# Kernel tuning notes

Hardware: AMD Instinct MI355X
Metric: run time of the kernel (lower is better)

The kernel has to match this reference:

```python
import jax, jax.numpy as jnp
import numpy as np

# dims: batch B, seq T, model C, expert hidden H, num experts E, top-k K
B, T, C, H, E, K = 4, 1024, 1024, 1024, 8, 2


def _swiglu(x):
    a, b = jnp.split(x, 2, axis=-1)
    return jax.nn.silu(a) * b


def setup_inputs() -> dict:
    key = jax.random.key(0)
    ks = jax.random.split(key, 6)
    s = 0.02
    x = jax.random.normal(ks[0], (B, T, C), jnp.float32)
    # weights stored [in, out] (transpose of torch Linear layout; same math y = x @ W)
    w_shared_in = jax.random.normal(ks[1], (C, 2 * H), jnp.float32) * s
    w_shared_out = jax.random.normal(ks[2], (H, C), jnp.float32) * s
    w1_shared = jax.random.normal(ks[3], (C, 2 * H), jnp.float32) * s
    w2 = jax.random.normal(ks[4], (E, H, C), jnp.float32) * s  # stacked routed_w2
    w_gate = jax.random.normal(ks[5], (C, E), jnp.float32) * s
    gate_bias = jnp.zeros((E,), jnp.float32)  # buffer, updated only in training
    return {
        "x": x,
        "w_shared_in": w_shared_in,
        "w_shared_out": w_shared_out,
        "w1_shared": w1_shared,
        "w2": w2,
        "w_gate": w_gate,
        "gate_bias": gate_bias,
    }


def reference(x, w_shared_in, w_shared_out, w1_shared, w2, w_gate, gate_bias):
    Bx, Tx, Cx = x.shape
    S = Bx * Tx
    fx = x.reshape(S, Cx)  # [S, C]

    # shared expert: SwiGLU MLP
    shared_out = _swiglu(fx @ w_shared_in) @ w_shared_out  # [S, C]

    # router: softmax(top-k) over biased logits
    logits = fx @ w_gate + gate_bias  # [S, E]
    probs = jax.nn.softmax(logits, axis=-1)
    top_val, top_idx = jax.lax.top_k(probs, K)  # [S, K]

    # dense dispatch-weight matrix [S, E] (zero where expert not selected)
    wdense = jnp.zeros((S, E), probs.dtype).at[
        jnp.arange(S)[:, None], top_idx
    ].add(top_val)

    # routed experts share w1_shared, so the SwiGLU hidden is identical for all
    # experts; compute it once for every token, then apply per-expert w2.
    hid = _swiglu(fx @ w1_shared)  # [S, H]
    routed_out = jnp.zeros_like(shared_out)
    for e in range(E):  # small fixed expert count
        routed_out = routed_out + wdense[:, e:e + 1] * (hid @ w2[e])

    return (shared_out + routed_out).reshape(Bx, Tx, Cx)
```

## Files before the change

kernel.cpp:

```cpp
#include <hip/hip_runtime.h>
#include <stdint.h>

typedef __attribute__((ext_vector_type(4))) float f32x4;
typedef __attribute__((ext_vector_type(8))) short s16x8;

static constexpr int S_TOK = 4096;
static constexpr int CDIM  = 1024;
static constexpr int HDIM  = 1024;
static constexpr int H2    = 2048;
static constexpr int NEXP  = 8;

#define BK 32
#define MAXRT2 40

__device__ __forceinline__ unsigned short f2bf(float f) {
  union { float f; uint32_t u; } c; c.f = f;
  uint32_t u = c.u;
  u += 0x7fffu + ((u >> 16) & 1u);
  return (unsigned short)(u >> 16);
}

__device__ __forceinline__ float bf2f(unsigned short u) {
  return __uint_as_float(((uint32_t)u) << 16);
}

__device__ __forceinline__ void gload16(const void* g, void* l) {
  __builtin_amdgcn_global_load_lds(
      (const __attribute__((address_space(1))) void*)g,
      (__attribute__((address_space(3))) void*)l, 16, 0, 0);
}

__global__ void cast_bf16_kernel(const float* __restrict__ src,
                                 unsigned short* __restrict__ dst, int n4) {
  int i = blockIdx.x * blockDim.x + threadIdx.x;
  const int st = gridDim.x * blockDim.x;
  for (; i < n4; i += st) {
    float4 v = reinterpret_cast<const float4*>(src)[i];
    ushort4 o;
    o.x = f2bf(v.x); o.y = f2bf(v.y); o.z = f2bf(v.z); o.w = f2bf(v.w);
    reinterpret_cast<ushort4*>(dst)[i] = o;
  }
}

__global__ void wprep_in_kernel(const float* __restrict__ wsi, const float* __restrict__ w1s,
                                unsigned short* __restrict__ dst) {
  __shared__ float t[32][33];
  const float* src = blockIdx.z ? w1s : wsi;
  const int halfoff = blockIdx.z ? 2048 : 0;
  const int r0 = blockIdx.y * 32;
  const int c0 = blockIdx.x * 32;
  const int tid = threadIdx.x;
#pragma unroll
  for (int i = 0; i < 4; ++i) {
    int idx = tid + i * 256;
    int r = idx >> 5, c = idx & 31;
    t[r][c] = src[(size_t)(r0 + r) * H2 + c0 + c];
  }
  __syncthreads();
#pragma unroll
  for (int i = 0; i < 4; ++i) {
    int idx = tid + i * 256;
    int r = idx >> 5, c = idx & 31;
    const int ccol = c0 + r;
    const int part = ccol >> 10, h = ccol & 1023;
    const int drow = halfoff + (h & 15) + ((h >> 4) << 5) + (part << 4);
    dst[(size_t)drow * CDIM + r0 + c] = f2bf(t[c][r]);
  }
}

__global__ void transpose_cast_kernel(const float* __restrict__ src,
                                      unsigned short* __restrict__ dst,
                                      int R, int Cc) {
  __shared__ float t[32][33];
  const size_t zoff = (size_t)blockIdx.z * R * Cc;
  src += zoff; dst += zoff;
  const int r0 = blockIdx.y * 32;
  const int c0 = blockIdx.x * 32;
  const int tid = threadIdx.x;
#pragma unroll
  for (int i = 0; i < 4; ++i) {
    int idx = tid + i * 256;
    int r = idx >> 5, c = idx & 31;
    t[r][c] = src[(size_t)(r0 + r) * Cc + c0 + c];
  }
  __syncthreads();
#pragma unroll
  for (int i = 0; i < 4; ++i) {
    int idx = tid + i * 256;
    int r = idx >> 5, c = idx & 31;
    dst[(size_t)(c0 + r) * R + r0 + c] = f2bf(t[c][r]);
  }
}

__global__ void router_kernel(const float* __restrict__ x, const float* __restrict__ wg,
                              const float* __restrict__ gb,
                              int2* __restrict__ ti_e, float2* __restrict__ ti_w) {
  const int l = threadIdx.x & 63;
  const int wid = threadIdx.x >> 6;
  const int s = blockIdx.x * 4 + wid;
  const float* xr = x + (size_t)s * CDIM;
  float acc[NEXP];
#pragma unroll
  for (int e = 0; e < NEXP; ++e) acc[e] = 0.f;
  for (int c = l; c < CDIM; c += 64) {
    float xv = xr[c];
    const float* wr_ = wg + (size_t)c * NEXP;
#pragma unroll
    for (int e = 0; e < NEXP; ++e) acc[e] += xv * wr_[e];
  }
#pragma unroll
  for (int e = 0; e < NEXP; ++e) {
#pragma unroll
    for (int off = 32; off > 0; off >>= 1) acc[e] += __shfl_xor(acc[e], off);
    acc[e] += gb[e];
  }
  float m = acc[0];
#pragma unroll
  for (int e = 1; e < NEXP; ++e) m = fmaxf(m, acc[e]);
  float ex[NEXP], sum = 0.f;
#pragma unroll
  for (int e = 0; e < NEXP; ++e) { ex[e] = __expf(acc[e] - m); sum += ex[e]; }
  int i0 = 0;
#pragma unroll
  for (int e = 1; e < NEXP; ++e) if (acc[e] > acc[i0]) i0 = e;
  int i1 = (i0 == 0) ? 1 : 0;
#pragma unroll
  for (int e = 0; e < NEXP; ++e) {
    if (e == i0) continue;
    if (acc[e] > acc[i1]) i1 = e;
  }
  if (l == 0) {
    const float inv = 1.f / sum;
    ti_e[s] = make_int2(i0, i1);
    ti_w[s] = make_float2(ex[i0] * inv, ex[i1] * inv);
  }
}

__global__ __launch_bounds__(1024) void build_kernel(
    const int2* __restrict__ ti_e,
    int* __restrict__ cnt, int* __restrict__ offs,
    int* __restrict__ gidx, int2* __restrict__ ti_slot) {
  __shared__ int gcnt[64][NEXP];
  __shared__ int gbase[64][NEXP];
  __shared__ int eoff[NEXP];
  const int tid = threadIdx.x;
  const int wid = tid >> 6, lane = tid & 63;

  for (int p = 0; p < 4; ++p) {
    const int g = p * 16 + wid;
    const int2 e = ti_e[g * 64 + lane];
#pragma unroll
    for (int ex = 0; ex < NEXP; ++ex) {
      uint64_t b0 = __ballot(e.x == ex);
      uint64_t b1 = __ballot(e.y == ex);
      if (lane == 0) gcnt[g][ex] = __popcll(b0) + __popcll(b1);
    }
  }
  __syncthreads();
  if (tid < NEXP) {
    const int ex = tid;
    int a = 0;
    for (int g = 0; g < 64; ++g) { gbase[g][ex] = a; a += gcnt[g][ex]; }
    eoff[ex] = a;
  }
  __syncthreads();
  if (tid == 0) {
    int a = 0;
#pragma unroll
    for (int ex = 0; ex < NEXP; ++ex) {
      const int c = eoff[ex];
      offs[ex] = a; cnt[ex] = c; eoff[ex] = a; a += c;
    }
    offs[NEXP] = a;
  }
  __syncthreads();
  for (int p = 0; p < 4; ++p) {
    const int g = p * 16 + wid;
    const int s = g * 64 + lane;
    const int2 e = ti_e[s];
    const uint64_t below = (lane == 0) ? 0ull : (~0ull >> (64 - lane));
    const uint64_t beloweq = below | (1ull << lane);
    int slot0 = 0, slot1 = 0;
#pragma unroll
    for (int ex = 0; ex < NEXP; ++ex) {
      uint64_t b0 = __ballot(e.x == ex);
      uint64_t b1 = __ballot(e.y == ex);
      const int base = gbase[g][ex];
      if (e.x == ex) slot0 = base + __popcll(b0 & below) + __popcll(b1 & below);
      if (e.y == ex) slot1 = base + __popcll(b0 & beloweq) + __popcll(b1 & below);
    }
    ti_slot[s] = make_int2(slot0, slot1);
    gidx[eoff[e.x] + slot0] = s;
    gidx[eoff[e.y] + slot1] = s;
  }
}

__global__ __launch_bounds__(256, 4) void gemm1_kernel(
    const unsigned short* __restrict__ xb, const unsigned short* __restrict__ w12i,
    unsigned short* __restrict__ Hs, unsigned short* __restrict__ Hr) {
  __shared__ unsigned short As[128 * BK];
  __shared__ unsigned short Bs[128 * BK];
  const int tid = threadIdx.x;
  const int l = tid & 63, wid = tid >> 6;
  const int wr = wid >> 1, wc = wid & 1;
  const int lr = l & 15, lk = (l >> 4) << 3;
  const int hw = blockIdx.y * gridDim.x + blockIdx.x;
  const int logical = (hw & 7) * 128 + (hw >> 3);
  const int m0 = (logical >> 5) * 128;
  const int n0 = (logical & 31) * 128;
  f32x4 acc[4][4] = {};
  const unsigned short* ga0 = xb + (size_t)(m0 + (tid >> 2)) * CDIM + ((tid & 3) << 3);
  const unsigned short* ga1 = ga0 + (size_t)64 * CDIM;
  const unsigned short* gb0 = w12i + (size_t)(n0 + (tid >> 2)) * CDIM + ((tid & 3) << 3);
  const unsigned short* gb1 = gb0 + (size_t)64 * CDIM;

  for (int k0 = 0; k0 < 1024; k0 += BK) {
    gload16(ga0 + k0, As + tid * 8);
    gload16(ga1 + k0, As + 2048 + tid * 8);
    gload16(gb0 + k0, Bs + tid * 8);
    gload16(gb1 + k0, Bs + 2048 + tid * 8);
    __syncthreads();
    s16x8 a[4], b[4];
#pragma unroll
    for (int fm = 0; fm < 4; ++fm)
      a[fm] = *reinterpret_cast<const s16x8*>(As + (wr * 64 + fm * 16 + lr) * BK + lk);
#pragma unroll
    for (int fn = 0; fn < 4; ++fn)
      b[fn] = *reinterpret_cast<const s16x8*>(Bs + (wc * 64 + fn * 16 + lr) * BK + lk);
#pragma unroll
    for (int fm = 0; fm < 4; ++fm)
#pragma unroll
      for (int fn = 0; fn < 4; ++fn)
        acc[fm][fn] = __builtin_amdgcn_mfma_f32_16x16x32_bf16(a[fm], b[fn], acc[fm][fn], 0, 0, 0);
    __syncthreads();
  }

  unsigned short* Hbuf = (n0 < 2048) ? Hs : Hr;
  const int rb = m0 + wr * 64 + ((l >> 4) << 2);
  const int hb0 = ((n0 & 2047) >> 1) + wc * 32;
#pragma unroll
  for (int fm = 0; fm < 4; ++fm)
#pragma unroll
    for (int j = 0; j < 2; ++j)
#pragma unroll
      for (int r = 0; r < 4; ++r) {
        float a = acc[fm][2 * j][r];
        float b = acc[fm][2 * j + 1][r];
        float hv = (a / (1.f + __expf(-a))) * b;
        Hbuf[(size_t)(rb + fm * 16 + r) * HDIM + hb0 + j * 16 + lr] = f2bf(hv);
      }
}

__global__ __launch_bounds__(512) void gemm2_kernel(
    const unsigned short* __restrict__ Hs, const unsigned short* __restrict__ Hr,
    const unsigned short* __restrict__ wso_t, const unsigned short* __restrict__ w2t,
    const int* __restrict__ cnt, const int* __restrict__ offs, const int* __restrict__ gidx,
    float* __restrict__ out, unsigned short* __restrict__ Eout) {
  __shared__ unsigned short SA[4][2][4096];
  __shared__ unsigned short SB[4][2][4096];
  const int tid = threadIdx.x;
  const int l = tid & 63, wid = tid >> 6;
  const int wm = wid >> 2, wn = wid & 3;
  const int lr = l & 15;
  const int hi8 = (l >> 4) << 3;
  const int wnh = wn >> 1;
  const int wno = (wn & 1) << 6;
  const int hw = blockIdx.y * gridDim.x + blockIdx.x;
  const int logical = (hw & 7) * 28 + (hw >> 3);
  const int gx = logical >> 2;
  const int n0 = (logical & 3) * 256;
  f32x4 acc[8][4] = {};

  const int srow = tid >> 2;
  const int cs = (((tid & 3) ^ ((tid >> 3) & 3)) << 3);

  const unsigned short *pa0, *pa1, *pb0, *pb1;
  int e = 0, cnte = 0, mt = 0, base = 0;
  const bool dense = (gx < 16);
  if (dense) {
    const int m0 = gx * 256;
    pa0 = Hs + (size_t)(m0 + srow) * HDIM + cs;
    pa1 = pa0 + (size_t)128 * HDIM;
    pb0 = wso_t + (size_t)(n0 + srow) * HDIM + cs;
    pb1 = pb0 + (size_t)128 * HDIM;
  } else {
    int t = gx - 16;
    bool found = false;
#pragma unroll
    for (int ee = 0; ee < NEXP; ++ee) {
      int c = cnt[ee];
      int nt = (c + 255) >> 8;
      if (!found) {
        if (t < nt) { e = ee; cnte = c; found = true; }
        else t -= nt;
      }
    }
    if (!found) return;
    mt = t;
    base = offs[e];
    const int r0 = mt * 256 + srow;
    const int tok0 = gidx[base + min(r0, cnte - 1)];
    const int tok1 = gidx[base + min(r0 + 128, cnte - 1)];
    pa0 = Hr + (size_t)tok0 * HDIM + cs;
    pa1 = Hr + (size_t)tok1 * HDIM + cs;
    pb0 = w2t + (size_t)e * CDIM * HDIM + (size_t)(n0 + srow) * HDIM + cs;
    pb1 = pb0 + (size_t)128 * HDIM;
  }

  const int t8 = tid * 8;
#pragma unroll
  for (int s = 0; s < 3; ++s) {
    const int kk = s * 32;
    gload16(pa0 + kk, &SA[s][0][t8]);
    gload16(pa1 + kk, &SA[s][1][t8]);
    gload16(pb0 + kk, &SB[s][0][t8]);
    gload16(pb1 + kk, &SB[s][1][t8]);
  }

  for (int s = 0; s < 32; ++s) {
    if (s < 30)       asm volatile("s_waitcnt vmcnt(8)" ::: "memory");
    else if (s == 30) asm volatile("s_waitcnt vmcnt(4)" ::: "memory");
    else              asm volatile("s_waitcnt vmcnt(0)" ::: "memory");
    __builtin_amdgcn_s_barrier();
    asm volatile("" ::: "memory");
    const int c = s & 3;
    const unsigned short* A_ = &SA[c][wm][0];
    const unsigned short* B_ = &SB[c][wnh][0];
    s16x8 a[8], b[4];
#pragma unroll
    for (int f = 0; f < 8; ++f) {
      const int r = f * 16 + lr;
      a[f] = *reinterpret_cast<const s16x8*>(&A_[r * 32 + (hi8 ^ (((r >> 1) & 3) << 3))]);
    }
#pragma unroll
    for (int j = 0; j < 4; ++j) {
      const int r = wno + j * 16 + lr;
      b[j] = *reinterpret_cast<const s16x8*>(&B_[r * 32 + (hi8 ^ (((r >> 1) & 3) << 3))]);
    }
    const int c3 = (s + 3) & 3;
    const int kk = (s + 3) * 32;
    const bool st = (s <= 28);
    if (st) gload16(pa0 + kk, &SA[c3][0][t8]);
    __builtin_amdgcn_s_setprio(1);
#pragma unroll
    for (int f = 0; f < 4; ++f) {
      acc[f][0] = __builtin_amdgcn_mfma_f32_16x16x32_bf16(a[f], b[0], acc[f][0], 0, 0, 0);
      acc[f][1] = __builtin_amdgcn_mfma_f32_16x16x32_bf16(a[f], b[1], acc[f][1], 0, 0, 0);
    }
    __builtin_amdgcn_s_setprio(0);
    if (st) gload16(pa1 + kk, &SA[c3][1][t8]);
    __builtin_amdgcn_s_setprio(1);
#pragma unroll
    for (int f = 0; f < 4; ++f) {
      acc[f][2] = __builtin_amdgcn_mfma_f32_16x16x32_bf16(a[f], b[2], acc[f][2], 0, 0, 0);
      acc[f][3] = __builtin_amdgcn_mfma_f32_16x16x32_bf16(a[f], b[3], acc[f][3], 0, 0, 0);
    }
    __builtin_amdgcn_s_setprio(0);
    if (st) gload16(pb0 + kk, &SB[c3][0][t8]);
    __builtin_amdgcn_s_setprio(1);
#pragma unroll
    for (int f = 0; f < 4; ++f) {
      acc[4 + f][0] = __builtin_amdgcn_mfma_f32_16x16x32_bf16(a[4 + f], b[0], acc[4 + f][0], 0, 0, 0);
      acc[4 + f][1] = __builtin_amdgcn_mfma_f32_16x16x32_bf16(a[4 + f], b[1], acc[4 + f][1], 0, 0, 0);
    }
    __builtin_amdgcn_s_setprio(0);
    if (st) gload16(pb1 + kk, &SB[c3][1][t8]);
    __builtin_amdgcn_s_setprio(1);
#pragma unroll
    for (int f = 0; f < 4; ++f) {
      acc[4 + f][2] = __builtin_amdgcn_mfma_f32_16x16x32_bf16(a[4 + f], b[2], acc[4 + f][2], 0, 0, 0);
      acc[4 + f][3] = __builtin_amdgcn_mfma_f32_16x16x32_bf16(a[4 + f], b[3], acc[4 + f][3], 0, 0, 0);
    }
    __builtin_amdgcn_s_setprio(0);
  }

  const int rloc0 = wm * 128 + ((l >> 4) << 2);
  const int cb = n0 + wn * 64 + lr;
  if (dense) {
    const int rb = gx * 256 + rloc0;
#pragma unroll
    for (int fm = 0; fm < 8; ++fm)
#pragma unroll
      for (int fn = 0; fn < 4; ++fn)
#pragma unroll
        for (int r = 0; r < 4; ++r)
          out[(size_t)(rb + fm * 16 + r) * CDIM + cb + fn * 16] = acc[fm][fn][r];
  } else {
#pragma unroll
    for (int fm = 0; fm < 8; ++fm)
#pragma unroll
      for (int fn = 0; fn < 4; ++fn)
#pragma unroll
        for (int r = 0; r < 4; ++r) {
          const int rloc = mt * 256 + rloc0 + fm * 16 + r;
          if (rloc < cnte)
            Eout[(size_t)(base + rloc) * CDIM + cb + fn * 16] = f2bf(acc[fm][fn][r]);
        }
  }
}

__global__ void scatter_kernel(float* __restrict__ out, const unsigned short* __restrict__ Eout,
                               const int2* __restrict__ ti_e, const int2* __restrict__ ti_slot,
                               const float2* __restrict__ ti_w, const int* __restrict__ offs) {
  const int total = S_TOK * (CDIM / 8);
  int i = blockIdx.x * blockDim.x + threadIdx.x;
  const int st = gridDim.x * blockDim.x;
  for (; i < total; i += st) {
    const int s = i >> 7;
    const int j = (i & 127) << 3;
    const int2 e = ti_e[s];
    const int2 sl = ti_slot[s];
    const float2 wv = ti_w[s];
    const int p0 = offs[e.x] + sl.x;
    const int p1 = offs[e.y] + sl.y;
    const ushort4* e0 = reinterpret_cast<const ushort4*>(Eout + (size_t)p0 * CDIM + j);
    const ushort4* e1 = reinterpret_cast<const ushort4*>(Eout + (size_t)p1 * CDIM + j);
    float* op = out + (size_t)s * CDIM + j;
#pragma unroll
    for (int q = 0; q < 2; ++q) {
      ushort4 a = e0[q], b = e1[q];
      float4 o = reinterpret_cast<float4*>(op)[q];
      o.x += wv.x * bf2f(a.x) + wv.y * bf2f(b.x);
      o.y += wv.x * bf2f(a.y) + wv.y * bf2f(b.y);
      o.z += wv.x * bf2f(a.z) + wv.y * bf2f(b.z);
      o.w += wv.x * bf2f(a.w) + wv.y * bf2f(b.w);
      reinterpret_cast<float4*>(op)[q] = o;
    }
  }
}

extern "C" void kernel_launch(void* const* d_in, const int* in_sizes, int n_in,
                              void* d_out, int out_size, void* d_ws, size_t ws_size,
                              hipStream_t stream) {
  (void)in_sizes; (void)n_in; (void)out_size; (void)ws_size;
  const float* x   = (const float*)d_in[0];
  const float* wsi = (const float*)d_in[1];
  const float* wso = (const float*)d_in[2];
  const float* w1s = (const float*)d_in[3];
  const float* w2  = (const float*)d_in[4];
  const float* wg  = (const float*)d_in[5];
  const float* gb  = (const float*)d_in[6];
  float* out = (float*)d_out;

  char* w = (char*)d_ws;
  auto alloc = [&](size_t bytes) {
    char* p = w; w += (bytes + 255) & ~(size_t)255; return p;
  };
  unsigned short* xb    = (unsigned short*)alloc((size_t)S_TOK * CDIM * 2);
  unsigned short* w12i  = (unsigned short*)alloc((size_t)2 * H2 * CDIM * 2);
  unsigned short* wso_t = (unsigned short*)alloc((size_t)CDIM * HDIM * 2);
  unsigned short* w2t   = (unsigned short*)alloc((size_t)NEXP * CDIM * HDIM * 2);
  unsigned short* Hs    = (unsigned short*)alloc((size_t)S_TOK * HDIM * 2);
  unsigned short* Hr    = (unsigned short*)alloc((size_t)S_TOK * HDIM * 2);
  unsigned short* Eout  = (unsigned short*)alloc((size_t)2 * S_TOK * CDIM * 2);
  int2*   ti_e   = (int2*)alloc((size_t)S_TOK * 8);
  int2*   ti_slot= (int2*)alloc((size_t)S_TOK * 8);
  float2* ti_w   = (float2*)alloc((size_t)S_TOK * 8);
  int*    cnt    = (int*)alloc(64);
  int*    offs   = (int*)alloc(64);
  int*    gidx   = (int*)alloc((size_t)2 * S_TOK * 4);

  router_kernel<<<S_TOK / 4, 256, 0, stream>>>(x, wg, gb, ti_e, ti_w);
  build_kernel<<<1, 1024, 0, stream>>>(ti_e, cnt, offs, gidx, ti_slot);

  cast_bf16_kernel<<<2048, 256, 0, stream>>>(x, xb, S_TOK * CDIM / 4);
  wprep_in_kernel<<<dim3(H2 / 32, CDIM / 32, 2), 256, 0, stream>>>(wsi, w1s, w12i);
  transpose_cast_kernel<<<dim3(CDIM / 32, HDIM / 32, 1), 256, 0, stream>>>(wso, wso_t, HDIM, CDIM);
  transpose_cast_kernel<<<dim3(CDIM / 32, HDIM / 32, NEXP), 256, 0, stream>>>(w2, w2t, HDIM, CDIM);

  gemm1_kernel<<<dim3(32, 32), 256, 0, stream>>>(xb, w12i, Hs, Hr);

  gemm2_kernel<<<dim3(16 + MAXRT2, CDIM / 256), 512, 0, stream>>>(
      Hs, Hr, wso_t, w2t, cnt, offs, gidx, out, Eout);

  scatter_kernel<<<2048, 256, 0, stream>>>(out, Eout, ti_e, ti_slot, ti_w, offs);
}
```

Measured before the change: 128.7 us.

## Fuse x cast into router, merge weight prep kernels, store shared output as bf16

The x-to-bf16 cast now happens inside the router kernel, which reads x with float4 loads, so x is read once instead of twice. The three weight transpose/cast kernels are merged into one flat-grid prep kernel to cut launch count. The shared-expert GEMM result is written to a bf16 buffer instead of fp32 out, so scatter writes out without first reading it. This trades less memory traffic and fewer launches for an extra bf16 rounding on the shared-expert output.

```diff
diff --git a/kernel.cpp b/kernel.cpp
--- a/kernel.cpp
+++ b/kernel.cpp
@@ -10,7 +10,6 @@
 static constexpr int H2    = 2048;
 static constexpr int NEXP  = 8;
 
-#define BK 32
 #define MAXRT2 40
 
 __device__ __forceinline__ unsigned short f2bf(float f) {
@@ -30,83 +29,93 @@
       (__attribute__((address_space(3))) void*)l, 16, 0, 0);
 }
 
-__global__ void cast_bf16_kernel(const float* __restrict__ src,
-                                 unsigned short* __restrict__ dst, int n4) {
-  int i = blockIdx.x * blockDim.x + threadIdx.x;
-  const int st = gridDim.x * blockDim.x;
-  for (; i < n4; i += st) {
-    float4 v = reinterpret_cast<const float4*>(src)[i];
-    ushort4 o;
-    o.x = f2bf(v.x); o.y = f2bf(v.y); o.z = f2bf(v.z); o.w = f2bf(v.w);
-    reinterpret_cast<ushort4*>(dst)[i] = o;
-  }
-}
-
-__global__ void wprep_in_kernel(const float* __restrict__ wsi, const float* __restrict__ w1s,
-                                unsigned short* __restrict__ dst) {
+__global__ __launch_bounds__(256) void prep_kernel(
+    const float* __restrict__ wsi, const float* __restrict__ w1s,
+    const float* __restrict__ wso, const float* __restrict__ w2,
+    unsigned short* __restrict__ w12i, unsigned short* __restrict__ wso_t,
+    unsigned short* __restrict__ w2t) {
   __shared__ float t[32][33];
-  const float* src = blockIdx.z ? w1s : wsi;
-  const int halfoff = blockIdx.z ? 2048 : 0;
-  const int r0 = blockIdx.y * 32;
-  const int c0 = blockIdx.x * 32;
+  const int b = blockIdx.x;
   const int tid = threadIdx.x;
+
+  if (b < 4096) {
+    const float* src = (b >= 2048) ? w1s : wsi;
+    const int halfoff = (b >= 2048) ? 2048 : 0;
+    const int rem = b & 2047;
+    const int r0 = (rem >> 6) * 32;
+    const int c0 = (rem & 63) * 32;
+#pragma unroll
+    for (int i = 0; i < 4; ++i) {
+      int idx = tid + i * 256;
+      int r = idx >> 5, c = idx & 31;
+      t[r][c] = src[(size_t)(r0 + r) * H2 + c0 + c];
+    }
+    __syncthreads();
+#pragma unroll
+    for (int i = 0; i < 4; ++i) {
+      int idx = tid + i * 256;
+      int r = idx >> 5, c = idx & 31;
+      const int ccol = c0 + r;
+      const int part = ccol >> 10, h = ccol & 1023;
+      const int drow = halfoff + (h & 15) + ((h >> 4) << 5) + (part << 4);
+      w12i[(size_t)drow * CDIM + r0 + c] = f2bf(t[c][r]);
+    }
+    return;
+  }
+  const float* src;
+  unsigned short* dst;
+  int bx, by;
+  if (b < 5120) {
+    const int b3 = b - 4096;
+    src = wso; dst = wso_t; by = b3 >> 5; bx = b3 & 31;
+  } else {
+    const int b4 = b - 5120;
+    const int z = b4 >> 10;
+    const int rem = b4 & 1023;
+    src = w2 + (size_t)z * HDIM * CDIM;
+    dst = w2t + (size_t)z * HDIM * CDIM;
+    by = rem >> 5; bx = rem & 31;
+  }
+  const int r0 = by * 32, c0 = bx * 32;
 #pragma unroll
   for (int i = 0; i < 4; ++i) {
     int idx = tid + i * 256;
     int r = idx >> 5, c = idx & 31;
-    t[r][c] = src[(size_t)(r0 + r) * H2 + c0 + c];
+    t[r][c] = src[(size_t)(r0 + r) * CDIM + c0 + c];
   }
   __syncthreads();
 #pragma unroll
   for (int i = 0; i < 4; ++i) {
     int idx = tid + i * 256;
     int r = idx >> 5, c = idx & 31;
-    const int ccol = c0 + r;
-    const int part = ccol >> 10, h = ccol & 1023;
-    const int drow = halfoff + (h & 15) + ((h >> 4) << 5) + (part << 4);
-    dst[(size_t)drow * CDIM + r0 + c] = f2bf(t[c][r]);
-  }
-}
-
-__global__ void transpose_cast_kernel(const float* __restrict__ src,
-                                      unsigned short* __restrict__ dst,
-                                      int R, int Cc) {
-  __shared__ float t[32][33];
-  const size_t zoff = (size_t)blockIdx.z * R * Cc;
-  src += zoff; dst += zoff;
-  const int r0 = blockIdx.y * 32;
-  const int c0 = blockIdx.x * 32;
-  const int tid = threadIdx.x;
-#pragma unroll
-  for (int i = 0; i < 4; ++i) {
-    int idx = tid + i * 256;
-    int r = idx >> 5, c = idx & 31;
-    t[r][c] = src[(size_t)(r0 + r) * Cc + c0 + c];
-  }
-  __syncthreads();
-#pragma unroll
-  for (int i = 0; i < 4; ++i) {
-    int idx = tid + i * 256;
-    int r = idx >> 5, c = idx & 31;
-    dst[(size_t)(c0 + r) * R + r0 + c] = f2bf(t[c][r]);
+    dst[(size_t)(c0 + r) * HDIM + r0 + c] = f2bf(t[c][r]);
   }
 }
 
 __global__ void router_kernel(const float* __restrict__ x, const float* __restrict__ wg,
                               const float* __restrict__ gb,
-                              int2* __restrict__ ti_e, float2* __restrict__ ti_w) {
+                              int2* __restrict__ ti_e, float2* __restrict__ ti_w,
+                              unsigned short* __restrict__ xb) {
   const int l = threadIdx.x & 63;
   const int wid = threadIdx.x >> 6;
   const int s = blockIdx.x * 4 + wid;
   const float* xr = x + (size_t)s * CDIM;
+  unsigned short* xbr = xb + (size_t)s * CDIM;
   float acc[NEXP];
 #pragma unroll
   for (int e = 0; e < NEXP; ++e) acc[e] = 0.f;
-  for (int c = l; c < CDIM; c += 64) {
-    float xv = xr[c];
-    const float* wr_ = wg + (size_t)c * NEXP;
-#pragma unroll
-    for (int e = 0; e < NEXP; ++e) acc[e] += xv * wr_[e];
+#pragma unroll
+  for (int c4 = 0; c4 < CDIM / 4; c4 += 64) {
+    const int i4 = c4 + l;
+    const float4 xv = reinterpret_cast<const float4*>(xr)[i4];
+    ushort4 o;
+    o.x = f2bf(xv.x); o.y = f2bf(xv.y); o.z = f2bf(xv.z); o.w = f2bf(xv.w);
+    reinterpret_cast<ushort4*>(xbr)[i4] = o;
+    const float* wr_ = wg + (size_t)i4 * 4 * NEXP;
+#pragma unroll
+    for (int e = 0; e < NEXP; ++e)
+      acc[e] += xv.x * wr_[e] + xv.y * wr_[e + NEXP] +
+                xv.z * wr_[e + 2 * NEXP] + xv.w * wr_[e + 3 * NEXP];
   }
 #pragma unroll
   for (int e = 0; e < NEXP; ++e) {
@@ -198,8 +207,8 @@
 __global__ __launch_bounds__(256, 4) void gemm1_kernel(
     const unsigned short* __restrict__ xb, const unsigned short* __restrict__ w12i,
     unsigned short* __restrict__ Hs, unsigned short* __restrict__ Hr) {
-  __shared__ unsigned short As[128 * BK];
-  __shared__ unsigned short Bs[128 * BK];
+  __shared__ unsigned short As[128 * 32];
+  __shared__ unsigned short Bs[128 * 32];
   const int tid = threadIdx.x;
   const int l = tid & 63, wid = tid >> 6;
   const int wr = wid >> 1, wc = wid & 1;
@@ -214,7 +223,7 @@
   const unsigned short* gb0 = w12i + (size_t)(n0 + (tid >> 2)) * CDIM + ((tid & 3) << 3);
   const unsigned short* gb1 = gb0 + (size_t)64 * CDIM;
 
-  for (int k0 = 0; k0 < 1024; k0 += BK) {
+  for (int k0 = 0; k0 < 1024; k0 += 32) {
     gload16(ga0 + k0, As + tid * 8);
     gload16(ga1 + k0, As + 2048 + tid * 8);
     gload16(gb0 + k0, Bs + tid * 8);
@@ -223,10 +232,10 @@
     s16x8 a[4], b[4];
 #pragma unroll
     for (int fm = 0; fm < 4; ++fm)
-      a[fm] = *reinterpret_cast<const s16x8*>(As + (wr * 64 + fm * 16 + lr) * BK + lk);
+      a[fm] = *reinterpret_cast<const s16x8*>(As + (wr * 64 + fm * 16 + lr) * 32 + lk);
 #pragma unroll
     for (int fn = 0; fn < 4; ++fn)
-      b[fn] = *reinterpret_cast<const s16x8*>(Bs + (wc * 64 + fn * 16 + lr) * BK + lk);
+      b[fn] = *reinterpret_cast<const s16x8*>(Bs + (wc * 64 + fn * 16 + lr) * 32 + lk);
 #pragma unroll
     for (int fm = 0; fm < 4; ++fm)
 #pragma unroll
@@ -255,7 +264,7 @@
     const unsigned short* __restrict__ Hs, const unsigned short* __restrict__ Hr,
     const unsigned short* __restrict__ wso_t, const unsigned short* __restrict__ w2t,
     const int* __restrict__ cnt, const int* __restrict__ offs, const int* __restrict__ gidx,
-    float* __restrict__ out, unsigned short* __restrict__ Eout) {
+    unsigned short* __restrict__ Dout, unsigned short* __restrict__ Eout) {
   __shared__ unsigned short SA[4][2][4096];
   __shared__ unsigned short SB[4][2][4096];
   const int tid = threadIdx.x;
@@ -384,7 +393,7 @@
       for (int fn = 0; fn < 4; ++fn)
 #pragma unroll
         for (int r = 0; r < 4; ++r)
-          out[(size_t)(rb + fm * 16 + r) * CDIM + cb + fn * 16] = acc[fm][fn][r];
+          Dout[(size_t)(rb + fm * 16 + r) * CDIM + cb + fn * 16] = f2bf(acc[fm][fn][r]);
   } else {
 #pragma unroll
     for (int fm = 0; fm < 8; ++fm)
@@ -399,7 +408,8 @@
   }
 }
 
-__global__ void scatter_kernel(float* __restrict__ out, const unsigned short* __restrict__ Eout,
+__global__ void scatter_kernel(float* __restrict__ out, const unsigned short* __restrict__ Dout,
+                               const unsigned short* __restrict__ Eout,
                                const int2* __restrict__ ti_e, const int2* __restrict__ ti_slot,
                                const float2* __restrict__ ti_w, const int* __restrict__ offs) {
   const int total = S_TOK * (CDIM / 8);
@@ -413,17 +423,18 @@
     const float2 wv = ti_w[s];
     const int p0 = offs[e.x] + sl.x;
     const int p1 = offs[e.y] + sl.y;
+    const ushort4* d0 = reinterpret_cast<const ushort4*>(Dout + (size_t)s * CDIM + j);
     const ushort4* e0 = reinterpret_cast<const ushort4*>(Eout + (size_t)p0 * CDIM + j);
     const ushort4* e1 = reinterpret_cast<const ushort4*>(Eout + (size_t)p1 * CDIM + j);
     float* op = out + (size_t)s * CDIM + j;
 #pragma unroll
     for (int q = 0; q < 2; ++q) {
-      ushort4 a = e0[q], b = e1[q];
-      float4 o = reinterpret_cast<float4*>(op)[q];
-      o.x += wv.x * bf2f(a.x) + wv.y * bf2f(b.x);
-      o.y += wv.x * bf2f(a.y) + wv.y * bf2f(b.y);
-      o.z += wv.x * bf2f(a.z) + wv.y * bf2f(b.z);
-      o.w += wv.x * bf2f(a.w) + wv.y * bf2f(b.w);
+      ushort4 dd = d0[q], a = e0[q], b = e1[q];
+      float4 o;
+      o.x = bf2f(dd.x) + wv.x * bf2f(a.x) + wv.y * bf2f(b.x);
+      o.y = bf2f(dd.y) + wv.x * bf2f(a.y) + wv.y * bf2f(b.y);
+      o.z = bf2f(dd.z) + wv.x * bf2f(a.z) + wv.y * bf2f(b.z);
+      o.w = bf2f(dd.w) + wv.x * bf2f(a.w) + wv.y * bf2f(b.w);
       reinterpret_cast<float4*>(op)[q] = o;
     }
   }
@@ -452,6 +463,7 @@
   unsigned short* w2t   = (unsigned short*)alloc((size_t)NEXP * CDIM * HDIM * 2);
   unsigned short* Hs    = (unsigned short*)alloc((size_t)S_TOK * HDIM * 2);
   unsigned short* Hr    = (unsigned short*)alloc((size_t)S_TOK * HDIM * 2);
+  unsigned short* Dout  = (unsigned short*)alloc((size_t)S_TOK * CDIM * 2);
   unsigned short* Eout  = (unsigned short*)alloc((size_t)2 * S_TOK * CDIM * 2);
   int2*   ti_e   = (int2*)alloc((size_t)S_TOK * 8);
   int2*   ti_slot= (int2*)alloc((size_t)S_TOK * 8);
@@ -460,18 +472,15 @@
   int*    offs   = (int*)alloc(64);
   int*    gidx   = (int*)alloc((size_t)2 * S_TOK * 4);
 
-  router_kernel<<<S_TOK / 4, 256, 0, stream>>>(x, wg, gb, ti_e, ti_w);
+  router_kernel<<<S_TOK / 4, 256, 0, stream>>>(x, wg, gb, ti_e, ti_w, xb);
   build_kernel<<<1, 1024, 0, stream>>>(ti_e, cnt, offs, gidx, ti_slot);
 
-  cast_bf16_kernel<<<2048, 256, 0, stream>>>(x, xb, S_TOK * CDIM / 4);
-  wprep_in_kernel<<<dim3(H2 / 32, CDIM / 32, 2), 256, 0, stream>>>(wsi, w1s, w12i);
-  transpose_cast_kernel<<<dim3(CDIM / 32, HDIM / 32, 1), 256, 0, stream>>>(wso, wso_t, HDIM, CDIM);
-  transpose_cast_kernel<<<dim3(CDIM / 32, HDIM / 32, NEXP), 256, 0, stream>>>(w2, w2t, HDIM, CDIM);
+  prep_kernel<<<13312, 256, 0, stream>>>(wsi, w1s, wso, w2, w12i, wso_t, w2t);
 
   gemm1_kernel<<<dim3(32, 32), 256, 0, stream>>>(xb, w12i, Hs, Hr);
 
   gemm2_kernel<<<dim3(16 + MAXRT2, CDIM / 256), 512, 0, stream>>>(
-      Hs, Hr, wso_t, w2t, cnt, offs, gidx, out, Eout);
-
-  scatter_kernel<<<2048, 256, 0, stream>>>(out, Eout, ti_e, ti_slot, ti_w, offs);
-}
+      Hs, Hr, wso_t, w2t, cnt, offs, gidx, Dout, Eout);
+
+  scatter_kernel<<<2048, 256, 0, stream>>>(out, Dout, Eout, ti_e, ti_slot, ti_w, offs);
+}
```

Measured after the change: 128.3 us. Within noise of the previous version (-0.3%).
